# Kernel tuning notes

Measured on AMD Instinct MI355X. Metric: run time of the kernel, lower is better.

The kernel has to match this reference:

```python
import jax, jax.numpy as jnp
import numpy as np

HIDDEN = 512
IN_FEAT = 512
BATCH = 64
SEQ = 1024


def setup_inputs() -> dict:
    key = jax.random.key(0)
    k1, k2, k3, k4 = jax.random.split(key, 4)
    x = jax.random.normal(k1, (BATCH, SEQ, IN_FEAT), dtype=jnp.float32)
    c0 = jnp.zeros((BATCH, HIDDEN), dtype=jnp.float32)
    h0 = jnp.zeros((BATCH, HIDDEN), dtype=jnp.float32)
    # Fused LSTM parameters (flax OptimizedLSTMCell layout: gates concatenated as i,f,g,o)
    scale_i = 1.0 / np.sqrt(IN_FEAT)
    scale_h = 1.0 / np.sqrt(HIDDEN)
    Wi = jax.random.normal(k2, (IN_FEAT, 4 * HIDDEN), dtype=jnp.float32) * scale_i
    Wh = jax.random.normal(k3, (HIDDEN, 4 * HIDDEN), dtype=jnp.float32) * scale_h
    b = jnp.zeros((4 * HIDDEN,), dtype=jnp.float32)
    return {"x": x, "c0": c0, "h0": h0, "Wi": Wi, "Wh": Wh, "b": b}


def reference(x, c0, h0, Wi, Wh, b):
    # Faithful to flax OptimizedLSTMCell scanned over time (axis 1):
    #   y = x_t @ Wi + h @ Wh + b ; i,f,g,o = split(y,4)
    #   c' = sigmoid(f)*c + sigmoid(i)*tanh(g) ; h' = sigmoid(o)*tanh(c')
    def step(carry, xt):
        c, h = carry
        y = xt @ Wi + h @ Wh + b  # [B, 4H]
        i, f, g, o = jnp.split(y, 4, axis=-1)
        new_c = jax.nn.sigmoid(f) * c + jax.nn.sigmoid(i) * jnp.tanh(g)
        new_h = jax.nn.sigmoid(o) * jnp.tanh(new_c)
        return (new_c, new_h), new_h

    xs = jnp.swapaxes(x, 0, 1)  # [T, B, D] for lax.scan
    (cT, hT), ys = jax.lax.scan(step, (c0, h0), xs)
    ys = jnp.swapaxes(ys, 0, 1)  # back to [B, T, H] (out_axes=1)
    return cT, hT, ys
```

## Files before the change

### kernel.cpp

```cpp
#include <hip/hip_runtime.h>
#include <hip/hip_fp16.h>


typedef _Float16 f16x8 __attribute__((ext_vector_type(8)));
typedef _Float16 f16x4 __attribute__((ext_vector_type(4)));
typedef float    f32x4 __attribute__((ext_vector_type(4)));

__device__ __forceinline__ float sigmoid_f(float v) {
    return 1.f / (1.f + __expf(-v));
}
__device__ __forceinline__ float tanh_f(float v) {
    v = fminf(15.f, fmaxf(-15.f, v));
    const float e = __expf(2.f * v);
    return (e - 1.f) / (e + 1.f);
}

__global__ __launch_bounds__(256, 1)
void lstm_persistent(const float* __restrict__ x,
                     const float* __restrict__ c0,
                     const float* __restrict__ h0,
                     const float* __restrict__ Wi,
                     const float* __restrict__ Wh,
                     const float* __restrict__ bias,
                     float* __restrict__ out,
                     unsigned* __restrict__ bar_base,
                     float* __restrict__ exch)
{
    const int bid  = blockIdx.x;
    const int cl   = (bid & 7) >> 1;
    const int wg   = ((bid >> 3) << 1) | (bid & 1);
    const int tid  = threadIdx.x;
    const int w    = tid >> 6;
    const int lane = tid & 63;
    const int q    = lane >> 4;
    const int n16  = lane & 15;

    const int gb0  = cl * 16;
    const int col0 = wg * 16;

    __shared__ _Float16 Alds[16 * 1024];
    __shared__ float    glds[4][16][17];

    unsigned* bar = bar_base + cl * 32;

    f16x8 Breg[32];
    {
        const int cg = w * 512 + col0 + n16;
#pragma unroll
        for (int kk = 0; kk < 32; ++kk) {
            const int kbase = kk * 32 + q * 8;
            f16x8 v;
#pragma unroll
            for (int j = 0; j < 8; ++j) {
                const int k = kbase + j;
                const float f = (k < 512) ? Wi[(size_t)k * 2048 + cg]
                                          : Wh[(size_t)(k - 512) * 2048 + cg];
                v[j] = (_Float16)f;
            }
            Breg[kk] = v;
        }
    }

    const int eb = tid >> 4;
    const int ej = tid & 15;
    const float bi_i = bias[0 * 512 + col0 + ej];
    const float bi_f = bias[1 * 512 + col0 + ej];
    const float bi_g = bias[2 * 512 + col0 + ej];
    const float bi_o = bias[3 * 512 + col0 + ej];
    float cst = c0[(size_t)(gb0 + eb) * 512 + col0 + ej];

    float4 xr[8];
#pragma unroll
    for (int cc = 0; cc < 8; ++cc) {
        const int chunk = tid + cc * 256;
        const int b  = chunk >> 7;
        const int k4 = chunk & 127;
        xr[cc] = *(const float4*)&x[((size_t)(gb0 + b) * 1024 + 0) * 512 + k4 * 4];
    }

    for (int t = 0; t < 1024; ++t) {
        if (t > 0) {
            if (tid == 0) {
                const unsigned target = 32u * (unsigned)t;
                int guard = 1 << 20;
                while (__hip_atomic_load(bar, __ATOMIC_ACQUIRE,
                                         __HIP_MEMORY_SCOPE_AGENT) < target) {
                    __builtin_amdgcn_s_sleep(1);
                    if (--guard == 0) break;
                }
            }
            __syncthreads();
        }

#pragma unroll
        for (int cc = 0; cc < 8; ++cc) {
            const int chunk = tid + cc * 256;
            const int b = chunk >> 7;
            const int k = (chunk & 127) * 4;
            f16x4 v;
            v[0] = (_Float16)xr[cc].x; v[1] = (_Float16)xr[cc].y;
            v[2] = (_Float16)xr[cc].z; v[3] = (_Float16)xr[cc].w;
            *(f16x4*)&Alds[b * 1024 + ((k + 8 * b) & 1023)] = v;
        }

        if (t == 0) {
#pragma unroll
            for (int cc = 0; cc < 4; ++cc) {
                const int chunk = tid + cc * 256;
                const int b  = chunk >> 6;
                const int k8 = chunk & 63;
                const float4 a0 = *(const float4*)&h0[(size_t)(gb0 + b) * 512 + k8 * 8];
                const float4 a1 = *(const float4*)&h0[(size_t)(gb0 + b) * 512 + k8 * 8 + 4];
                f16x8 v;
                v[0]=(_Float16)a0.x; v[1]=(_Float16)a0.y; v[2]=(_Float16)a0.z; v[3]=(_Float16)a0.w;
                v[4]=(_Float16)a1.x; v[5]=(_Float16)a1.y; v[6]=(_Float16)a1.z; v[7]=(_Float16)a1.w;
                *(f16x8*)&Alds[b * 1024 + ((512 + k8 * 8 + 8 * b) & 1023)] = v;
            }
        } else {
            const unsigned long long* src =
                (const unsigned long long*)(exch + (size_t)(t & 1) * (64 * 512));
#pragma unroll
            for (int cc = 0; cc < 4; ++cc) {
                const int chunk = tid + cc * 256;
                const int b  = chunk >> 6;
                const int k8 = chunk & 63;
                const int idx = ((gb0 + b) * 512 + k8 * 8) >> 1;
                union { unsigned long long u; float f[2]; } u0, u1, u2, u3;
                u0.u = __hip_atomic_load(&src[idx + 0], __ATOMIC_RELAXED, __HIP_MEMORY_SCOPE_AGENT);
                u1.u = __hip_atomic_load(&src[idx + 1], __ATOMIC_RELAXED, __HIP_MEMORY_SCOPE_AGENT);
                u2.u = __hip_atomic_load(&src[idx + 2], __ATOMIC_RELAXED, __HIP_MEMORY_SCOPE_AGENT);
                u3.u = __hip_atomic_load(&src[idx + 3], __ATOMIC_RELAXED, __HIP_MEMORY_SCOPE_AGENT);
                f16x8 v;
                v[0]=(_Float16)u0.f[0]; v[1]=(_Float16)u0.f[1];
                v[2]=(_Float16)u1.f[0]; v[3]=(_Float16)u1.f[1];
                v[4]=(_Float16)u2.f[0]; v[5]=(_Float16)u2.f[1];
                v[6]=(_Float16)u3.f[0]; v[7]=(_Float16)u3.f[1];
                *(f16x8*)&Alds[b * 1024 + ((512 + k8 * 8 + 8 * b) & 1023)] = v;
            }
        }
        __syncthreads();

        if (t < 1023) {
#pragma unroll
            for (int cc = 0; cc < 8; ++cc) {
                const int chunk = tid + cc * 256;
                const int b  = chunk >> 7;
                const int k4 = chunk & 127;
                xr[cc] = *(const float4*)&x[((size_t)(gb0 + b) * 1024 + (t + 1)) * 512 + k4 * 4];
            }
        }

        f32x4 acc0 = {0.f, 0.f, 0.f, 0.f}, acc1 = {0.f, 0.f, 0.f, 0.f};
        {
            const int m   = n16;
            const int rot = 8 * m;
#pragma unroll
            for (int kk = 0; kk < 32; kk += 2) {
                const int k0 = kk * 32 + q * 8;
                const f16x8 a0 = *(const f16x8*)&Alds[m * 1024 + ((k0      + rot) & 1023)];
                const f16x8 a1 = *(const f16x8*)&Alds[m * 1024 + ((k0 + 32 + rot) & 1023)];
                acc0 = __builtin_amdgcn_mfma_f32_16x16x32_f16(a0, Breg[kk],     acc0, 0, 0, 0);
                acc1 = __builtin_amdgcn_mfma_f32_16x16x32_f16(a1, Breg[kk + 1], acc1, 0, 0, 0);
            }
        }
#pragma unroll
        for (int r = 0; r < 4; ++r)
            glds[w][q * 4 + r][n16] = acc0[r] + acc1[r];
        __syncthreads();

        {
            const float yi = glds[0][eb][ej] + bi_i;
            const float yf = glds[1][eb][ej] + bi_f;
            const float yg = glds[2][eb][ej] + bi_g;
            const float yo = glds[3][eb][ej] + bi_o;
            cst = sigmoid_f(yf) * cst + sigmoid_f(yi) * tanh_f(yg);
            const float hn = sigmoid_f(yo) * tanh_f(cst);

            out[65536 + ((size_t)(gb0 + eb) * 1024 + t) * 512 + col0 + ej] = hn;
            if (t == 1023) {
                out[(size_t)(gb0 + eb) * 512 + col0 + ej]         = cst;
                out[32768 + (size_t)(gb0 + eb) * 512 + col0 + ej] = hn;
            }
            unsigned* dstu = (unsigned*)(exch + (size_t)((t + 1) & 1) * (64 * 512));
            __hip_atomic_store(&dstu[(gb0 + eb) * 512 + col0 + ej],
                               __float_as_uint(hn),
                               __ATOMIC_RELAXED, __HIP_MEMORY_SCOPE_AGENT);
        }
        __syncthreads();

        if (t < 1023 && tid == 0) {
            __hip_atomic_fetch_add(bar, 1u, __ATOMIC_ACQ_REL, __HIP_MEMORY_SCOPE_AGENT);
        }
    }
}

extern "C" void kernel_launch(void* const* d_in, const int* in_sizes, int n_in,
                              void* d_out, int out_size, void* d_ws, size_t ws_size,
                              hipStream_t stream) {
    const float* x  = (const float*)d_in[0];
    const float* c0 = (const float*)d_in[1];
    const float* h0 = (const float*)d_in[2];
    const float* Wi = (const float*)d_in[3];
    const float* Wh = (const float*)d_in[4];
    const float* b  = (const float*)d_in[5];
    float* out = (float*)d_out;

    hipMemsetAsync(d_ws, 0, 1024, stream);
    unsigned* bar = (unsigned*)d_ws;
    float* exch = (float*)((char*)d_ws + 1024);

    hipLaunchKernelGGL(lstm_persistent, dim3(128), dim3(256), 0, stream,
                       x, c0, h0, Wi, Wh, b, out, bar, exch);
}
```

Measured before the change: 5.828 ms.

## Replace atomic counter barrier with per-block flags and fp16 hidden exchange

```diff
diff --git a/kernel.cpp b/kernel.cpp
--- a/kernel.cpp
+++ b/kernel.cpp
@@ -23,8 +23,8 @@
                      const float* __restrict__ Wh,
                      const float* __restrict__ bias,
                      float* __restrict__ out,
-                     unsigned* __restrict__ bar_base,
-                     float* __restrict__ exch)
+                     unsigned* __restrict__ flags,
+                     _Float16* __restrict__ exch)
 {
     const int bid  = blockIdx.x;
     const int cl   = (bid & 7) >> 1;
@@ -38,10 +38,12 @@
     const int gb0  = cl * 16;
     const int col0 = wg * 16;
 
-    __shared__ _Float16 Alds[16 * 1024];
-    __shared__ float    glds[4][16][17];
-
-    unsigned* bar = bar_base + cl * 32;
+    __shared__ _Float16 Axl[16 * 512];
+    __shared__ float    glds[4][16][20];
+
+    unsigned* myflags = flags + cl * 32;
+    _Float16* exbuf0 = exch;
+    _Float16* exbuf1 = exch + 64 * 512;
 
     f16x8 Breg[32];
     {
@@ -75,71 +77,21 @@
         const int chunk = tid + cc * 256;
         const int b  = chunk >> 7;
         const int k4 = chunk & 127;
-        xr[cc] = *(const float4*)&x[((size_t)(gb0 + b) * 1024 + 0) * 512 + k4 * 4];
-    }
+        xr[cc] = *(const float4*)&x[(size_t)(gb0 + b) * 1024 * 512 + k4 * 4];
+    }
+#pragma unroll
+    for (int cc = 0; cc < 8; ++cc) {
+        const int chunk = tid + cc * 256;
+        const int b = chunk >> 7;
+        const int k = (chunk & 127) * 4;
+        f16x4 v;
+        v[0] = (_Float16)xr[cc].x; v[1] = (_Float16)xr[cc].y;
+        v[2] = (_Float16)xr[cc].z; v[3] = (_Float16)xr[cc].w;
+        *(f16x4*)&Axl[b * 512 + ((k + 8 * b) & 511)] = v;
+    }
+    __syncthreads();
 
     for (int t = 0; t < 1024; ++t) {
-        if (t > 0) {
-            if (tid == 0) {
-                const unsigned target = 32u * (unsigned)t;
-                int guard = 1 << 20;
-                while (__hip_atomic_load(bar, __ATOMIC_ACQUIRE,
-                                         __HIP_MEMORY_SCOPE_AGENT) < target) {
-                    __builtin_amdgcn_s_sleep(1);
-                    if (--guard == 0) break;
-                }
-            }
-            __syncthreads();
-        }
-
-#pragma unroll
-        for (int cc = 0; cc < 8; ++cc) {
-            const int chunk = tid + cc * 256;
-            const int b = chunk >> 7;
-            const int k = (chunk & 127) * 4;
-            f16x4 v;
-            v[0] = (_Float16)xr[cc].x; v[1] = (_Float16)xr[cc].y;
-            v[2] = (_Float16)xr[cc].z; v[3] = (_Float16)xr[cc].w;
-            *(f16x4*)&Alds[b * 1024 + ((k + 8 * b) & 1023)] = v;
-        }
-
-        if (t == 0) {
-#pragma unroll
-            for (int cc = 0; cc < 4; ++cc) {
-                const int chunk = tid + cc * 256;
-                const int b  = chunk >> 6;
-                const int k8 = chunk & 63;
-                const float4 a0 = *(const float4*)&h0[(size_t)(gb0 + b) * 512 + k8 * 8];
-                const float4 a1 = *(const float4*)&h0[(size_t)(gb0 + b) * 512 + k8 * 8 + 4];
-                f16x8 v;
-                v[0]=(_Float16)a0.x; v[1]=(_Float16)a0.y; v[2]=(_Float16)a0.z; v[3]=(_Float16)a0.w;
-                v[4]=(_Float16)a1.x; v[5]=(_Float16)a1.y; v[6]=(_Float16)a1.z; v[7]=(_Float16)a1.w;
-                *(f16x8*)&Alds[b * 1024 + ((512 + k8 * 8 + 8 * b) & 1023)] = v;
-            }
-        } else {
-            const unsigned long long* src =
-                (const unsigned long long*)(exch + (size_t)(t & 1) * (64 * 512));
-#pragma unroll
-            for (int cc = 0; cc < 4; ++cc) {
-                const int chunk = tid + cc * 256;
-                const int b  = chunk >> 6;
-                const int k8 = chunk & 63;
-                const int idx = ((gb0 + b) * 512 + k8 * 8) >> 1;
-                union { unsigned long long u; float f[2]; } u0, u1, u2, u3;
-                u0.u = __hip_atomic_load(&src[idx + 0], __ATOMIC_RELAXED, __HIP_MEMORY_SCOPE_AGENT);
-                u1.u = __hip_atomic_load(&src[idx + 1], __ATOMIC_RELAXED, __HIP_MEMORY_SCOPE_AGENT);
-                u2.u = __hip_atomic_load(&src[idx + 2], __ATOMIC_RELAXED, __HIP_MEMORY_SCOPE_AGENT);
-                u3.u = __hip_atomic_load(&src[idx + 3], __ATOMIC_RELAXED, __HIP_MEMORY_SCOPE_AGENT);
-                f16x8 v;
-                v[0]=(_Float16)u0.f[0]; v[1]=(_Float16)u0.f[1];
-                v[2]=(_Float16)u1.f[0]; v[3]=(_Float16)u1.f[1];
-                v[4]=(_Float16)u2.f[0]; v[5]=(_Float16)u2.f[1];
-                v[6]=(_Float16)u3.f[0]; v[7]=(_Float16)u3.f[1];
-                *(f16x8*)&Alds[b * 1024 + ((512 + k8 * 8 + 8 * b) & 1023)] = v;
-            }
-        }
-        __syncthreads();
-
         if (t < 1023) {
 #pragma unroll
             for (int cc = 0; cc < 8; ++cc) {
@@ -150,17 +102,60 @@
             }
         }
 
+        if (t > 0) {
+            if (lane < 32) {
+                const unsigned* f = myflags + lane;
+                const unsigned tgt = (unsigned)t;
+                int guard = 1 << 18;
+                while (__hip_atomic_load(f, __ATOMIC_RELAXED,
+                                         __HIP_MEMORY_SCOPE_AGENT) < tgt) {
+                    __builtin_amdgcn_s_sleep(1);
+                    if (--guard == 0) break;
+                }
+            }
+            __builtin_amdgcn_fence(__ATOMIC_ACQUIRE, "agent");
+        }
+
+        float4 hload[16];
+        if (t == 0) {
+            const float* hrow = h0 + (size_t)(gb0 + n16) * 512;
+#pragma unroll
+            for (int kk = 0; kk < 16; ++kk) {
+                const int k0 = kk * 32 + q * 8;
+                const float4 a0 = *(const float4*)&hrow[k0];
+                const float4 a1 = *(const float4*)&hrow[k0 + 4];
+                union { f16x8 h; float4 f; } u;
+                u.h[0]=(_Float16)a0.x; u.h[1]=(_Float16)a0.y;
+                u.h[2]=(_Float16)a0.z; u.h[3]=(_Float16)a0.w;
+                u.h[4]=(_Float16)a1.x; u.h[5]=(_Float16)a1.y;
+                u.h[6]=(_Float16)a1.z; u.h[7]=(_Float16)a1.w;
+                hload[kk] = u.f;
+            }
+        } else {
+            const _Float16* hrow = ((t & 1) ? exbuf1 : exbuf0) + (size_t)(gb0 + n16) * 512;
+#pragma unroll
+            for (int kk = 0; kk < 16; ++kk)
+                hload[kk] = *(const float4*)&hrow[kk * 32 + q * 8];
+        }
+
         f32x4 acc0 = {0.f, 0.f, 0.f, 0.f}, acc1 = {0.f, 0.f, 0.f, 0.f};
         {
             const int m   = n16;
             const int rot = 8 * m;
 #pragma unroll
-            for (int kk = 0; kk < 32; kk += 2) {
+            for (int kk = 0; kk < 16; kk += 2) {
                 const int k0 = kk * 32 + q * 8;
-                const f16x8 a0 = *(const f16x8*)&Alds[m * 1024 + ((k0      + rot) & 1023)];
-                const f16x8 a1 = *(const f16x8*)&Alds[m * 1024 + ((k0 + 32 + rot) & 1023)];
+                const f16x8 a0 = *(const f16x8*)&Axl[m * 512 + ((k0      + rot) & 511)];
+                const f16x8 a1 = *(const f16x8*)&Axl[m * 512 + ((k0 + 32 + rot) & 511)];
                 acc0 = __builtin_amdgcn_mfma_f32_16x16x32_f16(a0, Breg[kk],     acc0, 0, 0, 0);
                 acc1 = __builtin_amdgcn_mfma_f32_16x16x32_f16(a1, Breg[kk + 1], acc1, 0, 0, 0);
+            }
+#pragma unroll
+            for (int kk = 0; kk < 16; kk += 2) {
+                union { float4 f; f16x8 h; } u0, u1;
+                u0.f = hload[kk]; u1.f = hload[kk + 1];
+                acc0 = __builtin_amdgcn_mfma_f32_16x16x32_f16(u0.h, Breg[16 + kk],     acc0, 0, 0, 0);
+                acc1 = __builtin_amdgcn_mfma_f32_16x16x32_f16(u1.h, Breg[16 + kk + 1], acc1, 0, 0, 0);
             }
         }
 #pragma unroll
@@ -168,28 +163,46 @@
             glds[w][q * 4 + r][n16] = acc0[r] + acc1[r];
         __syncthreads();
 
-        {
-            const float yi = glds[0][eb][ej] + bi_i;
-            const float yf = glds[1][eb][ej] + bi_f;
-            const float yg = glds[2][eb][ej] + bi_g;
-            const float yo = glds[3][eb][ej] + bi_o;
-            cst = sigmoid_f(yf) * cst + sigmoid_f(yi) * tanh_f(yg);
-            const float hn = sigmoid_f(yo) * tanh_f(cst);
-
-            out[65536 + ((size_t)(gb0 + eb) * 1024 + t) * 512 + col0 + ej] = hn;
-            if (t == 1023) {
-                out[(size_t)(gb0 + eb) * 512 + col0 + ej]         = cst;
-                out[32768 + (size_t)(gb0 + eb) * 512 + col0 + ej] = hn;
-            }
-            unsigned* dstu = (unsigned*)(exch + (size_t)((t + 1) & 1) * (64 * 512));
-            __hip_atomic_store(&dstu[(gb0 + eb) * 512 + col0 + ej],
-                               __float_as_uint(hn),
-                               __ATOMIC_RELAXED, __HIP_MEMORY_SCOPE_AGENT);
+        const float yi = glds[0][eb][ej] + bi_i;
+        const float yf = glds[1][eb][ej] + bi_f;
+        const float yg = glds[2][eb][ej] + bi_g;
+        const float yo = glds[3][eb][ej] + bi_o;
+        cst = sigmoid_f(yf) * cst + sigmoid_f(yi) * tanh_f(yg);
+        const float hn = sigmoid_f(yo) * tanh_f(cst);
+
+        if (t < 1023) {
+            const _Float16 hf = (_Float16)hn;
+            unsigned ub;
+            { union { _Float16 h; unsigned short s; } c; c.h = hf; ub = c.s; }
+            const unsigned pb = __shfl_xor((int)ub, 1);
+            if ((ej & 1) == 0) {
+                _Float16* dstbuf = ((t & 1) ? exbuf0 : exbuf1);
+                unsigned* dst = (unsigned*)(dstbuf + (size_t)(gb0 + eb) * 512 + col0 + ej);
+                __hip_atomic_store(dst, ub | (pb << 16),
+                                   __ATOMIC_RELAXED, __HIP_MEMORY_SCOPE_AGENT);
+            }
+#pragma unroll
+            for (int cc = 0; cc < 8; ++cc) {
+                const int chunk = tid + cc * 256;
+                const int b = chunk >> 7;
+                const int k = (chunk & 127) * 4;
+                f16x4 v;
+                v[0] = (_Float16)xr[cc].x; v[1] = (_Float16)xr[cc].y;
+                v[2] = (_Float16)xr[cc].z; v[3] = (_Float16)xr[cc].w;
+                *(f16x4*)&Axl[b * 512 + ((k + 8 * b) & 511)] = v;
+            }
         }
         __syncthreads();
 
         if (t < 1023 && tid == 0) {
-            __hip_atomic_fetch_add(bar, 1u, __ATOMIC_ACQ_REL, __HIP_MEMORY_SCOPE_AGENT);
+            __hip_atomic_store(myflags + wg, (unsigned)(t + 1),
+                               __ATOMIC_RELEASE, __HIP_MEMORY_SCOPE_AGENT);
+        }
+
+        out[65536 + ((size_t)(gb0 + eb) * 1024 + t) * 512 + col0 + ej] = hn;
+        if (t == 1023) {
+            out[(size_t)(gb0 + eb) * 512 + col0 + ej]         = cst;
+            out[32768 + (size_t)(gb0 + eb) * 512 + col0 + ej] = hn;
         }
     }
 }
@@ -206,9 +219,9 @@
     float* out = (float*)d_out;
 
     hipMemsetAsync(d_ws, 0, 1024, stream);
-    unsigned* bar = (unsigned*)d_ws;
-    float* exch = (float*)((char*)d_ws + 1024);
+    unsigned* flags = (unsigned*)d_ws;
+    _Float16* exch  = (_Float16*)((char*)d_ws + 1024);
 
     hipLaunchKernelGGL(lstm_persistent, dim3(128), dim3(256), 0, stream,
-                       x, c0, h0, Wi, Wh, b, out, bar, exch);
-}
+                       x, c0, h0, Wi, Wh, b, out, flags, exch);
+}
```

After: 10.22 ms. +75.4%, slower.
